# Kernel optimization log

Hardware: AMD Instinct MI355X
Metric: run time of the kernel (lower is better)

The kernel has to match this reference:

```python
import jax, jax.numpy as jnp
import numpy as np

D_Q = 512
D_O = 256  # = d_v = d_k = d_o
N_HEAD = 8
BN_EPS = 1e-5
LEAK = 0.1


def setup_inputs() -> dict:
    key = jax.random.key(0)
    ks = jax.random.split(key, 8)
    s = 0.02
    inp = {
        "q": jax.random.normal(ks[0], (64, D_Q), dtype=jnp.float32),
        "v": jax.random.normal(ks[1], (64, D_O, 32, 32), dtype=jnp.float32),
        "w_q": jax.random.normal(ks[2], (D_O, D_Q), dtype=jnp.float32) * s,
        "b_q": jnp.zeros((D_O,), jnp.float32),
        "w_kc": jax.random.normal(ks[3], (D_O, D_O), dtype=jnp.float32) * s,
        "b_kc": jnp.zeros((D_O,), jnp.float32),
        "w_kd": jax.random.normal(ks[4], (D_O, D_O), dtype=jnp.float32) * s,
        "b_kd": jnp.zeros((D_O,), jnp.float32),
        "w_v": jax.random.normal(ks[5], (D_O, D_O), dtype=jnp.float32) * s,
        "b_v": jnp.zeros((D_O,), jnp.float32),
        "temp_c": jnp.asarray(1.0, jnp.float32),
        "temp_d": jnp.asarray(1.0, jnp.float32),
        "bn_gamma": jnp.ones((D_O,), jnp.float32),
        "bn_beta": jnp.zeros((D_O,), jnp.float32),
        "bn_mean": jnp.zeros((D_O,), jnp.float32),
        "bn_var": jnp.ones((D_O,), jnp.float32),
    }
    return inp


def _conv1x1(x, wgt, bias):
    # x: (b, c, h, w), wgt: (o, c) -> (b, o, h, w)
    return jnp.einsum('bchw,oc->bohw', x, wgt) + bias[None, :, None, None]


def reference(q, v, w_q, b_q, w_kc, b_kc, w_kd, b_kd, w_v, b_v,
              temp_c, temp_d, bn_gamma, bn_beta, bn_mean, bn_var):
    b = q.shape[0]
    _, c_v, h, w = v.shape
    n = N_HEAD
    dh = D_O // n
    hw = h * w
    residual = v

    # projections
    qv = (q @ w_q.T + b_q).reshape(b, n, dh)                      # (b, n, dh)
    kc = _conv1x1(v, w_kc, b_kc).reshape(b, n, dh, hw).transpose(0, 1, 3, 2)  # (b, n, hw, dh)
    kd = _conv1x1(v, w_kd, b_kd).reshape(b, n, dh, hw).transpose(0, 1, 3, 2)
    vp = _conv1x1(v, w_v, b_v).reshape(b, n, dh, hw).transpose(0, 1, 3, 2)

    # collect: softmax attention with query length 1
    col_logit = jnp.einsum('bnd,bnsd->bns', qv, kc) / temp_c      # (b, n, hw)
    attn_col = jax.nn.softmax(col_logit, axis=2)
    attn = jnp.einsum('bns,bnsd->bnd', attn_col, vp)              # (b, n, dh)

    # diffuse: sigmoid gate, outer product with collected vector
    dif = jax.nn.sigmoid(jnp.einsum('bnsd,bnd->bns', kd, qv) / temp_d)  # (b, n, hw)
    out = jnp.einsum('bns,bnd->bnsd', dif, attn)                  # (b, n, hw, dh)

    # faithful to torch permute(0,1,4,3,2).view: swaps h and w (requires h==w)
    out = out.reshape(b, n, h, w, dh).transpose(0, 1, 4, 3, 2).reshape(b, D_O, w, h)
    out = out + residual

    # BatchNorm2d (eval: running stats) + LeakyReLU(0.1); dropout is identity at eval
    inv = bn_gamma / jnp.sqrt(bn_var + BN_EPS)
    out = (out - bn_mean[None, :, None, None]) * inv[None, :, None, None] + bn_beta[None, :, None, None]
    out = jnp.where(out >= 0, out, LEAK * out)
    return out
```

## Files before the change

kernel.cpp:

```cpp
#include <hip/hip_runtime.h>
#include <math.h>

#define B    64
#define DQ   512
#define DO   256
#define NH   8
#define DH   32
#define HW   1024
#define NCH  4
#define CHS  256

__global__ __launch_bounds__(256) void k1_qv(const float* __restrict__ q,
                                             const float* __restrict__ w_q,
                                             const float* __restrict__ b_q,
                                             float* __restrict__ qv) {
    int cg = blockIdx.x, b = blockIdx.y;
    int t = threadIdx.x;
    int wid = t >> 6, lane = t & 63;
    const float4* qrow = reinterpret_cast<const float4*>(q + (size_t)b*DQ);
    float4 q0 = qrow[lane*2], q1 = qrow[lane*2 + 1];
    #pragma unroll
    for (int r = 0; r < 4; ++r) {
        int c = cg*16 + wid*4 + r;
        const float4* wrow = reinterpret_cast<const float4*>(w_q + (size_t)c*DQ);
        float4 w0 = wrow[lane*2], w1 = wrow[lane*2 + 1];
        float acc = q0.x*w0.x + q0.y*w0.y + q0.z*w0.z + q0.w*w0.w
                  + q1.x*w1.x + q1.y*w1.y + q1.z*w1.z + q1.w*w1.w;
        #pragma unroll
        for (int k = 32; k > 0; k >>= 1) acc += __shfl_xor(acc, k);
        if (lane == 0) qv[b*DO + c] = acc + b_q[c];
    }
}

__global__ void k2_wqk(const float* __restrict__ qv,
                       const float* __restrict__ w_kc, const float* __restrict__ b_kc,
                       const float* __restrict__ w_kd, const float* __restrict__ b_kd,
                       const float* __restrict__ temp_c, const float* __restrict__ temp_d,
                       float* __restrict__ wqkc, float* __restrict__ wqkd,
                       float* __restrict__ qbc, float* __restrict__ qbd) {
    int bn = blockIdx.x;
    int n  = bn & 7;
    int t  = threadIdx.x;
    __shared__ float qvs[DH];
    if (t < DH) qvs[t] = qv[(bn >> 3)*DO + n*DH + t];
    __syncthreads();
    float itc = 1.0f / temp_c[0];
    float itd = 1.0f / temp_d[0];
    float ac = 0.f, ad = 0.f;
    #pragma unroll
    for (int d = 0; d < DH; ++d) {
        float qd = qvs[d];
        ac += qd * w_kc[(n*DH + d)*DO + t];
        ad += qd * w_kd[(n*DH + d)*DO + t];
    }
    wqkc[bn*DO + t] = ac * itc;
    wqkd[bn*DO + t] = ad * itd;
    if (t == 0) {
        float sc = 0.f;
        for (int d = 0; d < DH; ++d) sc += qvs[d]*b_kc[n*DH + d];
        qbc[bn] = sc * itc;
    }
    if (t == 1) {
        float sd = 0.f;
        for (int d = 0; d < DH; ++d) sd += qvs[d]*b_kd[n*DH + d];
        qbd[bn] = sd * itd;
    }
}

__global__ __launch_bounds__(512)
void k3g(const float* __restrict__ v,
         const float* __restrict__ wqkc, const float* __restrict__ wqkd,
         const float* __restrict__ qbc,  const float* __restrict__ qbd,
         float* __restrict__ gate, float* __restrict__ pvp, float* __restrict__ mz) {
    __shared__ float e_lds[NH][CHS];
    int ch = blockIdx.x, b = blockIdx.y;
    int t  = threadIdx.x;
    int s0 = ch*CHS;
    int bn0 = b*NH;
    int lane = t & 63;
    int w = __builtin_amdgcn_readfirstlane(t >> 6);

    float ac0=0.f, ac1=0.f, ac2=0.f, ac3=0.f;
    float ad0=0.f, ad1=0.f, ad2=0.f, ad3=0.f;
    {
        const float* vb = v + (size_t)b*DO*HW + s0 + lane*4;
        const float* wc = wqkc + (size_t)(bn0 + w)*DO;
        const float* wd = wqkd + (size_t)(bn0 + w)*DO;
        #pragma unroll 8
        for (int c = 0; c < DO; ++c) {
            float4 v4 = *reinterpret_cast<const float4*>(vb + (size_t)c*HW);
            float wcv = wc[c];
            float wdv = wd[c];
            ac0 = fmaf(wcv, v4.x, ac0); ac1 = fmaf(wcv, v4.y, ac1);
            ac2 = fmaf(wcv, v4.z, ac2); ac3 = fmaf(wcv, v4.w, ac3);
            ad0 = fmaf(wdv, v4.x, ad0); ad1 = fmaf(wdv, v4.y, ad1);
            ad2 = fmaf(wdv, v4.z, ad2); ad3 = fmaf(wdv, v4.w, ad3);
        }
    }

    {
        float qc = qbc[bn0 + w], qd = qbd[bn0 + w];
        float g0 = 1.0f/(1.0f + __expf(-(ad0 + qd)));
        float g1 = 1.0f/(1.0f + __expf(-(ad1 + qd)));
        float g2 = 1.0f/(1.0f + __expf(-(ad2 + qd)));
        float g3 = 1.0f/(1.0f + __expf(-(ad3 + qd)));
        *reinterpret_cast<float4*>(gate + (size_t)(bn0 + w)*HW + s0 + lane*4)
            = make_float4(g0, g1, g2, g3);

        float l0 = ac0 + qc, l1 = ac1 + qc, l2 = ac2 + qc, l3 = ac3 + qc;
        float m = fmaxf(fmaxf(l0, l1), fmaxf(l2, l3));
        #pragma unroll
        for (int k = 32; k > 0; k >>= 1) m = fmaxf(m, __shfl_xor(m, k));
        float e0 = __expf(l0 - m), e1 = __expf(l1 - m), e2 = __expf(l2 - m), e3 = __expf(l3 - m);
        float z = e0 + e1 + e2 + e3;
        #pragma unroll
        for (int k = 32; k > 0; k >>= 1) z += __shfl_xor(z, k);
        *reinterpret_cast<float4*>(&e_lds[w][lane*4]) = make_float4(e0, e1, e2, e3);
        if (lane == 0) {
            float* mzp = mz + ((size_t)(b*NCH + ch)*NH + w)*2;
            mzp[0] = m; mzp[1] = z;
        }
    }
    __syncthreads();

    {
        int ng = t >> 8;
        int c  = t & 255;
        const float* vrow = v + ((size_t)(b*DO + c))*HW + s0;
        float a0 = 0.f, a1 = 0.f, a2 = 0.f, a3 = 0.f;
        #pragma unroll 4
        for (int j = 0; j < CHS/4; ++j) {
            float4 v4 = *reinterpret_cast<const float4*>(vrow + j*4);
            float4 e0 = *reinterpret_cast<const float4*>(&e_lds[ng*4+0][j*4]);
            float4 e1 = *reinterpret_cast<const float4*>(&e_lds[ng*4+1][j*4]);
            float4 e2 = *reinterpret_cast<const float4*>(&e_lds[ng*4+2][j*4]);
            float4 e3 = *reinterpret_cast<const float4*>(&e_lds[ng*4+3][j*4]);
            a0 += v4.x*e0.x + v4.y*e0.y + v4.z*e0.z + v4.w*e0.w;
            a1 += v4.x*e1.x + v4.y*e1.y + v4.z*e1.z + v4.w*e1.w;
            a2 += v4.x*e2.x + v4.y*e2.y + v4.z*e2.z + v4.w*e2.w;
            a3 += v4.x*e3.x + v4.y*e3.y + v4.z*e3.z + v4.w*e3.w;
        }
        size_t pb = ((size_t)(b*NCH + ch)*NH + ng*4)*DO + c;
        pvp[pb]        = a0;
        pvp[pb + DO]   = a1;
        pvp[pb + 2*DO] = a2;
        pvp[pb + 3*DO] = a3;
    }
}

__global__ void k4c(const float* __restrict__ pvp, const float* __restrict__ mz,
                    const float* __restrict__ w_v, const float* __restrict__ b_v,
                    float* __restrict__ attn) {
    __shared__ float scale[NCH][NH];
    __shared__ float pv_lds[NH*DO];
    int b = blockIdx.x, t = threadIdx.x;
    if (t < NH) {
        int n = t;
        float M = -1e30f;
        for (int ch = 0; ch < NCH; ++ch)
            M = fmaxf(M, mz[((size_t)(b*NCH+ch)*NH+n)*2]);
        float Z = 0.f;
        for (int ch = 0; ch < NCH; ++ch) {
            float sc = __expf(mz[((size_t)(b*NCH+ch)*NH+n)*2] - M);
            Z += sc * mz[((size_t)(b*NCH+ch)*NH+n)*2 + 1];
            scale[ch][n] = sc;
        }
        float inv = 1.0f/Z;
        for (int ch = 0; ch < NCH; ++ch) scale[ch][n] *= inv;
    }
    __syncthreads();
    #pragma unroll
    for (int r = 0; r < 2; ++r) {
        int i4 = t + r*256;
        int n  = i4 >> 6;
        float4 s = make_float4(0.f, 0.f, 0.f, 0.f);
        #pragma unroll
        for (int ch = 0; ch < NCH; ++ch) {
            float sc = scale[ch][n];
            float4 p = reinterpret_cast<const float4*>(pvp + (size_t)(b*NCH + ch)*NH*DO)[i4];
            s.x = fmaf(sc, p.x, s.x); s.y = fmaf(sc, p.y, s.y);
            s.z = fmaf(sc, p.z, s.z); s.w = fmaf(sc, p.w, s.w);
        }
        *reinterpret_cast<float4*>(&pv_lds[i4*4]) = s;
    }
    __syncthreads();
    int n = t >> 5;
    float acc = b_v[t];
    const float4* w4 = reinterpret_cast<const float4*>(w_v + t*DO);
    #pragma unroll 4
    for (int c4 = 0; c4 < DO/4; ++c4) {
        float4 wv = w4[c4];
        int c = c4*4;
        acc += pv_lds[n*DO+c]*wv.x + pv_lds[n*DO+c+1]*wv.y + pv_lds[n*DO+c+2]*wv.z + pv_lds[n*DO+c+3]*wv.w;
    }
    attn[b*DO + t] = acc;
}

__global__ void k5_out(const float* __restrict__ v, const float* __restrict__ gate,
                       const float* __restrict__ attn,
                       const float* __restrict__ bn_g, const float* __restrict__ bn_b,
                       const float* __restrict__ bn_m, const float* __restrict__ bn_v,
                       float* __restrict__ out) {
    int c = blockIdx.x, b = blockIdx.y;
    int n = c >> 5, d = c & 31;
    int t = threadIdx.x;
    __shared__ float g[32*33];
    float4 gv = reinterpret_cast<const float4*>(gate + (b*NH + n)*HW)[t];
    int s0 = t*4;
    int ga = s0 >> 5, gb = s0 & 31;
    g[ga*33 + gb + 0] = gv.x;
    g[ga*33 + gb + 1] = gv.y;
    g[ga*33 + gb + 2] = gv.z;
    g[ga*33 + gb + 3] = gv.w;
    __syncthreads();
    float av   = attn[(b*NH + n)*DH + d];
    float inv  = bn_g[c] / sqrtf(bn_v[c] + 1e-5f);
    float mean = bn_m[c], beta = bn_b[c];
    size_t base = ((size_t)(b*DO + c))*HW;
    float4 r4 = reinterpret_cast<const float4*>(v + base)[t];
    int l = 4*t;
    int i_ = l >> 5, j_ = l & 31;
    float x0 = g[(j_+0)*33 + i_]*av + r4.x;
    float x1 = g[(j_+1)*33 + i_]*av + r4.y;
    float x2 = g[(j_+2)*33 + i_]*av + r4.z;
    float x3 = g[(j_+3)*33 + i_]*av + r4.w;
    float y0 = (x0 - mean)*inv + beta; y0 = y0 >= 0.f ? y0 : 0.1f*y0;
    float y1 = (x1 - mean)*inv + beta; y1 = y1 >= 0.f ? y1 : 0.1f*y1;
    float y2 = (x2 - mean)*inv + beta; y2 = y2 >= 0.f ? y2 : 0.1f*y2;
    float y3 = (x3 - mean)*inv + beta; y3 = y3 >= 0.f ? y3 : 0.1f*y3;
    reinterpret_cast<float4*>(out + base)[t] = make_float4(y0, y1, y2, y3);
}

extern "C" void kernel_launch(void* const* d_in, const int* in_sizes, int n_in,
                              void* d_out, int out_size, void* d_ws, size_t ws_size,
                              hipStream_t stream) {
    const float* q      = (const float*)d_in[0];
    const float* v      = (const float*)d_in[1];
    const float* w_q    = (const float*)d_in[2];
    const float* b_q    = (const float*)d_in[3];
    const float* w_kc   = (const float*)d_in[4];
    const float* b_kc   = (const float*)d_in[5];
    const float* w_kd   = (const float*)d_in[6];
    const float* b_kd   = (const float*)d_in[7];
    const float* w_v    = (const float*)d_in[8];
    const float* b_v    = (const float*)d_in[9];
    const float* temp_c = (const float*)d_in[10];
    const float* temp_d = (const float*)d_in[11];
    const float* bn_g   = (const float*)d_in[12];
    const float* bn_b   = (const float*)d_in[13];
    const float* bn_m   = (const float*)d_in[14];
    const float* bn_v   = (const float*)d_in[15];
    float* out = (float*)d_out;

    float* ws   = (float*)d_ws;
    float* qv   = ws;
    float* wqkc = qv   + B*DO;
    float* wqkd = wqkc + B*NH*DO;
    float* qbc  = wqkd + B*NH*DO;
    float* qbd  = qbc  + B*NH;
    float* gate = qbd  + B*NH;
    float* mz   = gate + B*NH*HW;
    float* pvp  = mz   + B*NCH*NH*2;
    float* attn = pvp  + B*NCH*NH*DO;

    k1_qv <<<dim3(16, B),    256, 0, stream>>>(q, w_q, b_q, qv);
    k2_wqk<<<B*NH,           256, 0, stream>>>(qv, w_kc, b_kc, w_kd, b_kd, temp_c, temp_d,
                                               wqkc, wqkd, qbc, qbd);
    k3g   <<<dim3(NCH, B),   512, 0, stream>>>(v, wqkc, wqkd, qbc, qbd, gate, pvp, mz);
    k4c   <<<B,              256, 0, stream>>>(pvp, mz, w_v, b_v, attn);
    k5_out<<<dim3(DO, B),    256, 0, stream>>>(v, gate, attn, bn_g, bn_b, bn_m, bn_v, out);
}
```

Measured before the change: 82.91 us.

## Split channel reduction across waves in logit kernel and halve chunk size

The logit/gate kernel is reorganized so that each wave accumulates a 32-channel slice for all eight heads, instead of one head over all 256 channels. Partial sums go to LDS and are reduced per head before the sigmoid and softmax steps. This removes the eight-fold redundant reads of the v chunk within a block. Chunks shrink to 128 positions, doubling the grid, at the cost of about 68 KB of LDS per block, which limits how many blocks fit on a CU, plus an extra barrier.

```diff
diff --git a/kernel.cpp b/kernel.cpp
--- a/kernel.cpp
+++ b/kernel.cpp
@@ -7,8 +7,8 @@
 #define NH   8
 #define DH   32
 #define HW   1024
-#define NCH  4
-#define CHS  256
+#define NCH  8
+#define CHS  128
 
 __global__ __launch_bounds__(256) void k1_qv(const float* __restrict__ q,
                                              const float* __restrict__ w_q,
@@ -67,57 +67,76 @@
     }
 }
 
-__global__ __launch_bounds__(512)
-void k3g(const float* __restrict__ v,
+__global__ __launch_bounds__(512, 4)
+void k3h(const float* __restrict__ v,
          const float* __restrict__ wqkc, const float* __restrict__ wqkd,
          const float* __restrict__ qbc,  const float* __restrict__ qbd,
          float* __restrict__ gate, float* __restrict__ pvp, float* __restrict__ mz) {
+    __shared__ float pc[8*NH*CHS];
+    __shared__ float pd[8*NH*CHS];
     __shared__ float e_lds[NH][CHS];
     int ch = blockIdx.x, b = blockIdx.y;
     int t  = threadIdx.x;
     int s0 = ch*CHS;
     int bn0 = b*NH;
     int lane = t & 63;
-    int w = __builtin_amdgcn_readfirstlane(t >> 6);
-
-    float ac0=0.f, ac1=0.f, ac2=0.f, ac3=0.f;
-    float ad0=0.f, ad1=0.f, ad2=0.f, ad3=0.f;
+    int sl2  = lane*2;
+    int csub = __builtin_amdgcn_readfirstlane(t >> 6);
+
     {
-        const float* vb = v + (size_t)b*DO*HW + s0 + lane*4;
-        const float* wc = wqkc + (size_t)(bn0 + w)*DO;
-        const float* wd = wqkd + (size_t)(bn0 + w)*DO;
+        const float* vb = v + (size_t)b*DO*HW + s0 + sl2;
+        const float* wc = wqkc + (size_t)bn0*DO;
+        const float* wd = wqkd + (size_t)bn0*DO;
+        float acc_c0[NH] = {0,0,0,0,0,0,0,0}, acc_c1[NH] = {0,0,0,0,0,0,0,0};
+        float acc_d0[NH] = {0,0,0,0,0,0,0,0}, acc_d1[NH] = {0,0,0,0,0,0,0,0};
+        int cbase = csub*32;
         #pragma unroll 8
-        for (int c = 0; c < DO; ++c) {
-            float4 v4 = *reinterpret_cast<const float4*>(vb + (size_t)c*HW);
-            float wcv = wc[c];
-            float wdv = wd[c];
-            ac0 = fmaf(wcv, v4.x, ac0); ac1 = fmaf(wcv, v4.y, ac1);
-            ac2 = fmaf(wcv, v4.z, ac2); ac3 = fmaf(wcv, v4.w, ac3);
-            ad0 = fmaf(wdv, v4.x, ad0); ad1 = fmaf(wdv, v4.y, ad1);
-            ad2 = fmaf(wdv, v4.z, ad2); ad3 = fmaf(wdv, v4.w, ad3);
-        }
-    }
+        for (int cc = 0; cc < 32; ++cc) {
+            int c = cbase + cc;
+            float2 v2 = *reinterpret_cast<const float2*>(vb + (size_t)c*HW);
+            #pragma unroll
+            for (int n = 0; n < NH; ++n) {
+                float wcv = wc[n*DO + c];
+                float wdv = wd[n*DO + c];
+                acc_c0[n] = fmaf(wcv, v2.x, acc_c0[n]);
+                acc_c1[n] = fmaf(wcv, v2.y, acc_c1[n]);
+                acc_d0[n] = fmaf(wdv, v2.x, acc_d0[n]);
+                acc_d1[n] = fmaf(wdv, v2.y, acc_d1[n]);
+            }
+        }
+        #pragma unroll
+        for (int n = 0; n < NH; ++n) {
+            *reinterpret_cast<float2*>(&pc[(csub*NH + n)*CHS + sl2]) = make_float2(acc_c0[n], acc_c1[n]);
+            *reinterpret_cast<float2*>(&pd[(csub*NH + n)*CHS + sl2]) = make_float2(acc_d0[n], acc_d1[n]);
+        }
+    }
+    __syncthreads();
 
     {
-        float qc = qbc[bn0 + w], qd = qbd[bn0 + w];
-        float g0 = 1.0f/(1.0f + __expf(-(ad0 + qd)));
-        float g1 = 1.0f/(1.0f + __expf(-(ad1 + qd)));
-        float g2 = 1.0f/(1.0f + __expf(-(ad2 + qd)));
-        float g3 = 1.0f/(1.0f + __expf(-(ad3 + qd)));
-        *reinterpret_cast<float4*>(gate + (size_t)(bn0 + w)*HW + s0 + lane*4)
-            = make_float4(g0, g1, g2, g3);
-
-        float l0 = ac0 + qc, l1 = ac1 + qc, l2 = ac2 + qc, l3 = ac3 + qc;
-        float m = fmaxf(fmaxf(l0, l1), fmaxf(l2, l3));
+        int n = csub;
+        float lc0 = qbc[bn0+n], lc1 = lc0;
+        float ld0 = qbd[bn0+n], ld1 = ld0;
+        #pragma unroll
+        for (int k = 0; k < 8; ++k) {
+            float2 c2 = *reinterpret_cast<const float2*>(&pc[(k*NH + n)*CHS + sl2]);
+            float2 d2 = *reinterpret_cast<const float2*>(&pd[(k*NH + n)*CHS + sl2]);
+            lc0 += c2.x; lc1 += c2.y;
+            ld0 += d2.x; ld1 += d2.y;
+        }
+        float g0 = 1.0f/(1.0f + __expf(-ld0));
+        float g1 = 1.0f/(1.0f + __expf(-ld1));
+        *reinterpret_cast<float2*>(gate + (size_t)(bn0+n)*HW + s0 + sl2) = make_float2(g0, g1);
+
+        float m = fmaxf(lc0, lc1);
         #pragma unroll
         for (int k = 32; k > 0; k >>= 1) m = fmaxf(m, __shfl_xor(m, k));
-        float e0 = __expf(l0 - m), e1 = __expf(l1 - m), e2 = __expf(l2 - m), e3 = __expf(l3 - m);
-        float z = e0 + e1 + e2 + e3;
+        float e0 = __expf(lc0 - m), e1 = __expf(lc1 - m);
+        float z = e0 + e1;
         #pragma unroll
         for (int k = 32; k > 0; k >>= 1) z += __shfl_xor(z, k);
-        *reinterpret_cast<float4*>(&e_lds[w][lane*4]) = make_float4(e0, e1, e2, e3);
+        *reinterpret_cast<float2*>(&e_lds[n][sl2]) = make_float2(e0, e1);
         if (lane == 0) {
-            float* mzp = mz + ((size_t)(b*NCH + ch)*NH + w)*2;
+            float* mzp = mz + ((size_t)(b*NCH + ch)*NH + n)*2;
             mzp[0] = m; mzp[1] = z;
         }
     }
@@ -266,7 +285,7 @@
     k1_qv <<<dim3(16, B),    256, 0, stream>>>(q, w_q, b_q, qv);
     k2_wqk<<<B*NH,           256, 0, stream>>>(qv, w_kc, b_kc, w_kd, b_kd, temp_c, temp_d,
                                                wqkc, wqkd, qbc, qbd);
-    k3g   <<<dim3(NCH, B),   512, 0, stream>>>(v, wqkc, wqkd, qbc, qbd, gate, pvp, mz);
+    k3h   <<<dim3(NCH, B),   512, 0, stream>>>(v, wqkc, wqkd, qbc, qbd, gate, pvp, mz);
     k4c   <<<B,              256, 0, stream>>>(pvp, mz, w_v, b_v, attn);
     k5_out<<<dim3(DO, B),    256, 0, stream>>>(v, gate, attn, bn_g, bn_b, bn_m, bn_v, out);
 }
```

Measured after the change: 77.41 us. 1.07x faster.

## Stage v channel tiles through double-buffered LDS and split spatial chunks finer

Applied to the files above, without the earlier changes.

The logit kernel now splits each batch's spatial dimension into 16 chunks of 64 instead of 4 of 256, giving 1024 blocks instead of 256 so more blocks can occupy the GPU. Each block loads v in 32-channel tiles into a double-buffered shared-memory array and prefetches the next tile while computing on the current one, so each v element is read from global memory once per block instead of once per wave. Each thread now handles one spatial position rather than four. The cost is a barrier per channel tile, more partial results for k4c to combine, and a tighter launch bound that may limit registers.

```diff
diff --git a/kernel.cpp b/kernel.cpp
--- a/kernel.cpp
+++ b/kernel.cpp
@@ -7,8 +7,10 @@
 #define NH   8
 #define DH   32
 #define HW   1024
-#define NCH  4
-#define CHS  256
+#define NCH  16
+#define CHS  64
+#define CG   32
+#define NT   (DO/CG)
 
 __global__ __launch_bounds__(256) void k1_qv(const float* __restrict__ q,
                                              const float* __restrict__ w_q,
@@ -67,11 +69,12 @@
     }
 }
 
-__global__ __launch_bounds__(512)
-void k3g(const float* __restrict__ v,
+__global__ __launch_bounds__(512, 8)
+void k3i(const float* __restrict__ v,
          const float* __restrict__ wqkc, const float* __restrict__ wqkd,
          const float* __restrict__ qbc,  const float* __restrict__ qbd,
          float* __restrict__ gate, float* __restrict__ pvp, float* __restrict__ mz) {
+    __shared__ float buf[2][CG][CHS];
     __shared__ float e_lds[NH][CHS];
     int ch = blockIdx.x, b = blockIdx.y;
     int t  = threadIdx.x;
@@ -80,42 +83,47 @@
     int lane = t & 63;
     int w = __builtin_amdgcn_readfirstlane(t >> 6);
 
-    float ac0=0.f, ac1=0.f, ac2=0.f, ac3=0.f;
-    float ad0=0.f, ad1=0.f, ad2=0.f, ad3=0.f;
+    int srow = t >> 4, sc4 = (t & 15)*4;
+    const float* vb = v + (size_t)b*DO*HW + s0;
+
     {
-        const float* vb = v + (size_t)b*DO*HW + s0 + lane*4;
-        const float* wc = wqkc + (size_t)(bn0 + w)*DO;
-        const float* wd = wqkd + (size_t)(bn0 + w)*DO;
-        #pragma unroll 8
-        for (int c = 0; c < DO; ++c) {
-            float4 v4 = *reinterpret_cast<const float4*>(vb + (size_t)c*HW);
-            float wcv = wc[c];
-            float wdv = wd[c];
-            ac0 = fmaf(wcv, v4.x, ac0); ac1 = fmaf(wcv, v4.y, ac1);
-            ac2 = fmaf(wcv, v4.z, ac2); ac3 = fmaf(wcv, v4.w, ac3);
-            ad0 = fmaf(wdv, v4.x, ad0); ad1 = fmaf(wdv, v4.y, ad1);
-            ad2 = fmaf(wdv, v4.z, ad2); ad3 = fmaf(wdv, v4.w, ad3);
-        }
+        float4 st = *reinterpret_cast<const float4*>(vb + (size_t)srow*HW + sc4);
+        *reinterpret_cast<float4*>(&buf[0][srow][sc4]) = st;
+    }
+    __syncthreads();
+
+    float lc = qbc[bn0 + w];
+    float ld = qbd[bn0 + w];
+    const float* wcn = wqkc + (size_t)(bn0 + w)*DO;
+    const float* wdn = wqkd + (size_t)(bn0 + w)*DO;
+    #pragma unroll
+    for (int g = 0; g < NT; ++g) {
+        int cur = g & 1;
+        float4 nx;
+        if (g < NT-1)
+            nx = *reinterpret_cast<const float4*>(vb + (size_t)((g+1)*CG + srow)*HW + sc4);
+        int cbase = g*CG;
+        #pragma unroll
+        for (int cc = 0; cc < CG; ++cc) {
+            float vv = buf[cur][cc][lane];
+            lc = fmaf(wcn[cbase + cc], vv, lc);
+            ld = fmaf(wdn[cbase + cc], vv, ld);
+        }
+        if (g < NT-1)
+            *reinterpret_cast<float4*>(&buf[cur ^ 1][srow][sc4]) = nx;
+        __syncthreads();
     }
 
     {
-        float qc = qbc[bn0 + w], qd = qbd[bn0 + w];
-        float g0 = 1.0f/(1.0f + __expf(-(ad0 + qd)));
-        float g1 = 1.0f/(1.0f + __expf(-(ad1 + qd)));
-        float g2 = 1.0f/(1.0f + __expf(-(ad2 + qd)));
-        float g3 = 1.0f/(1.0f + __expf(-(ad3 + qd)));
-        *reinterpret_cast<float4*>(gate + (size_t)(bn0 + w)*HW + s0 + lane*4)
-            = make_float4(g0, g1, g2, g3);
-
-        float l0 = ac0 + qc, l1 = ac1 + qc, l2 = ac2 + qc, l3 = ac3 + qc;
-        float m = fmaxf(fmaxf(l0, l1), fmaxf(l2, l3));
+        gate[(size_t)(bn0 + w)*HW + s0 + lane] = 1.0f/(1.0f + __expf(-ld));
+        float m = lc;
         #pragma unroll
         for (int k = 32; k > 0; k >>= 1) m = fmaxf(m, __shfl_xor(m, k));
-        float e0 = __expf(l0 - m), e1 = __expf(l1 - m), e2 = __expf(l2 - m), e3 = __expf(l3 - m);
-        float z = e0 + e1 + e2 + e3;
+        float e = __expf(lc - m);
+        e_lds[w][lane] = e;
+        float z = e;
         #pragma unroll
         for (int k = 32; k > 0; k >>= 1) z += __shfl_xor(z, k);
-        *reinterpret_cast<float4*>(&e_lds[w][lane*4]) = make_float4(e0, e1, e2, e3);
         if (lane == 0) {
             float* mzp = mz + ((size_t)(b*NCH + ch)*NH + w)*2;
             mzp[0] = m; mzp[1] = z;
@@ -128,7 +136,7 @@
         int c  = t & 255;
         const float* vrow = v + ((size_t)(b*DO + c))*HW + s0;
         float a0 = 0.f, a1 = 0.f, a2 = 0.f, a3 = 0.f;
-        #pragma unroll 4
+        #pragma unroll
         for (int j = 0; j < CHS/4; ++j) {
             float4 v4 = *reinterpret_cast<const float4*>(vrow + j*4);
             float4 e0 = *reinterpret_cast<const float4*>(&e_lds[ng*4+0][j*4]);
@@ -266,7 +274,7 @@
     k1_qv <<<dim3(16, B),    256, 0, stream>>>(q, w_q, b_q, qv);
     k2_wqk<<<B*NH,           256, 0, stream>>>(qv, w_kc, b_kc, w_kd, b_kd, temp_c, temp_d,
                                                wqkc, wqkd, qbc, qbd);
-    k3g   <<<dim3(NCH, B),   512, 0, stream>>>(v, wqkc, wqkd, qbc, qbd, gate, pvp, mz);
+    k3i   <<<dim3(NCH, B),   512, 0, stream>>>(v, wqkc, wqkd, qbc, qbd, gate, pvp, mz);
     k4c   <<<B,              256, 0, stream>>>(pvp, mz, w_v, b_v, attn);
     k5_out<<<dim3(DO, B),    256, 0, stream>>>(v, gate, attn, bn_g, bn_b, bn_m, bn_v, out);
 }
```

New measurement: 81.26 us. 1.02x faster.

## Stage v chunk in swizzled LDS and split spatial axis into smaller chunks

Applied to the files above, without the earlier changes.

The main fused kernel now loads a 256x64 tile of v into shared memory once, with an XOR swizzle, and reuses it for both the key-logit and the value-accumulation passes. Before, v was read from global memory twice. The spatial chunk shrinks from 256 to 64 (16 chunks), which multiplies the block count by four so more CUs are busy. Each wave splits the channel loop across four lane groups and reduces them with shuffles. The two per-head weight vectors are interleaved into one float2 buffer. The cost is more partial results for the combine kernel and 72KB of LDS per block.

```diff
diff --git a/kernel.cpp b/kernel.cpp
--- a/kernel.cpp
+++ b/kernel.cpp
@@ -7,8 +7,8 @@
 #define NH   8
 #define DH   32
 #define HW   1024
-#define NCH  4
-#define CHS  256
+#define NCH  16
+#define CHS  64
 
 __global__ __launch_bounds__(256) void k1_qv(const float* __restrict__ q,
                                              const float* __restrict__ w_q,
@@ -36,13 +36,14 @@
                        const float* __restrict__ w_kc, const float* __restrict__ b_kc,
                        const float* __restrict__ w_kd, const float* __restrict__ b_kd,
                        const float* __restrict__ temp_c, const float* __restrict__ temp_d,
-                       float* __restrict__ wqkc, float* __restrict__ wqkd,
-                       float* __restrict__ qbc, float* __restrict__ qbd) {
+                       float* __restrict__ wpack, float* __restrict__ qbc,
+                       float* __restrict__ qbd) {
     int bn = blockIdx.x;
     int n  = bn & 7;
+    int bb = bn >> 3;
     int t  = threadIdx.x;
     __shared__ float qvs[DH];
-    if (t < DH) qvs[t] = qv[(bn >> 3)*DO + n*DH + t];
+    if (t < DH) qvs[t] = qv[bb*DO + n*DH + t];
     __syncthreads();
     float itc = 1.0f / temp_c[0];
     float itd = 1.0f / temp_d[0];
@@ -53,8 +54,8 @@
         ac += qd * w_kc[(n*DH + d)*DO + t];
         ad += qd * w_kd[(n*DH + d)*DO + t];
     }
-    wqkc[bn*DO + t] = ac * itc;
-    wqkd[bn*DO + t] = ad * itd;
+    wpack[((size_t)bn*DO + t)*2 + 0] = ac * itc;
+    wpack[((size_t)bn*DO + t)*2 + 1] = ad * itd;
     if (t == 0) {
         float sc = 0.f;
         for (int d = 0; d < DH; ++d) sc += qvs[d]*b_kc[n*DH + d];
@@ -67,11 +68,12 @@
     }
 }
 
-__global__ __launch_bounds__(512)
-void k3g(const float* __restrict__ v,
-         const float* __restrict__ wqkc, const float* __restrict__ wqkd,
+__global__ __launch_bounds__(512, 2)
+void k3r(const float* __restrict__ v,
+         const float* __restrict__ wpack,
          const float* __restrict__ qbc,  const float* __restrict__ qbd,
          float* __restrict__ gate, float* __restrict__ pvp, float* __restrict__ mz) {
+    __shared__ float vbuf[DO][CHS];
     __shared__ float e_lds[NH][CHS];
     int ch = blockIdx.x, b = blockIdx.y;
     int t  = threadIdx.x;
@@ -80,42 +82,65 @@
     int lane = t & 63;
     int w = __builtin_amdgcn_readfirstlane(t >> 6);
 
+    {
+        int s4 = t & 15, srow = t >> 4;
+        const float* vb = v + (size_t)b*DO*HW + s0;
+        int idx4 = (s4 ^ (srow & 15)) * 4;
+        #pragma unroll
+        for (int k = 0; k < 8; ++k) {
+            float4 r = *reinterpret_cast<const float4*>(vb + (size_t)(k*32+srow)*HW + s4*4);
+            *reinterpret_cast<float4*>(&vbuf[k*32+srow][idx4]) = r;
+        }
+    }
+    __syncthreads();
+
     float ac0=0.f, ac1=0.f, ac2=0.f, ac3=0.f;
     float ad0=0.f, ad1=0.f, ad2=0.f, ad3=0.f;
     {
-        const float* vb = v + (size_t)b*DO*HW + s0 + lane*4;
-        const float* wc = wqkc + (size_t)(bn0 + w)*DO;
-        const float* wd = wqkd + (size_t)(bn0 + w)*DO;
+        int c_off = lane >> 4, s4 = lane & 15;
+        const float2* wp = reinterpret_cast<const float2*>(wpack) + (size_t)(bn0 + w)*DO;
         #pragma unroll 8
-        for (int c = 0; c < DO; ++c) {
-            float4 v4 = *reinterpret_cast<const float4*>(vb + (size_t)c*HW);
-            float wcv = wc[c];
-            float wdv = wd[c];
-            ac0 = fmaf(wcv, v4.x, ac0); ac1 = fmaf(wcv, v4.y, ac1);
-            ac2 = fmaf(wcv, v4.z, ac2); ac3 = fmaf(wcv, v4.w, ac3);
-            ad0 = fmaf(wdv, v4.x, ad0); ad1 = fmaf(wdv, v4.y, ad1);
-            ad2 = fmaf(wdv, v4.z, ad2); ad3 = fmaf(wdv, v4.w, ad3);
-        }
-    }
-
-    {
+        for (int cc = 0; cc < 64; ++cc) {
+            int c = cc*4 + c_off;
+            float4 v4 = *reinterpret_cast<const float4*>(&vbuf[c][(s4 ^ (c & 15))*4]);
+            float2 wv = wp[c];
+            ac0 = fmaf(wv.x, v4.x, ac0); ac1 = fmaf(wv.x, v4.y, ac1);
+            ac2 = fmaf(wv.x, v4.z, ac2); ac3 = fmaf(wv.x, v4.w, ac3);
+            ad0 = fmaf(wv.y, v4.x, ad0); ad1 = fmaf(wv.y, v4.y, ad1);
+            ad2 = fmaf(wv.y, v4.z, ad2); ad3 = fmaf(wv.y, v4.w, ad3);
+        }
+        ac0 += __shfl_xor(ac0, 16); ac0 += __shfl_xor(ac0, 32);
+        ac1 += __shfl_xor(ac1, 16); ac1 += __shfl_xor(ac1, 32);
+        ac2 += __shfl_xor(ac2, 16); ac2 += __shfl_xor(ac2, 32);
+        ac3 += __shfl_xor(ac3, 16); ac3 += __shfl_xor(ac3, 32);
+        ad0 += __shfl_xor(ad0, 16); ad0 += __shfl_xor(ad0, 32);
+        ad1 += __shfl_xor(ad1, 16); ad1 += __shfl_xor(ad1, 32);
+        ad2 += __shfl_xor(ad2, 16); ad2 += __shfl_xor(ad2, 32);
+        ad3 += __shfl_xor(ad3, 16); ad3 += __shfl_xor(ad3, 32);
+    }
+
+    {
+        int s4 = lane & 15;
         float qc = qbc[bn0 + w], qd = qbd[bn0 + w];
+        float l0 = ac0 + qc, l1 = ac1 + qc, l2 = ac2 + qc, l3 = ac3 + qc;
         float g0 = 1.0f/(1.0f + __expf(-(ad0 + qd)));
         float g1 = 1.0f/(1.0f + __expf(-(ad1 + qd)));
         float g2 = 1.0f/(1.0f + __expf(-(ad2 + qd)));
         float g3 = 1.0f/(1.0f + __expf(-(ad3 + qd)));
-        *reinterpret_cast<float4*>(gate + (size_t)(bn0 + w)*HW + s0 + lane*4)
-            = make_float4(g0, g1, g2, g3);
-
-        float l0 = ac0 + qc, l1 = ac1 + qc, l2 = ac2 + qc, l3 = ac3 + qc;
+        if (lane < 16)
+            *reinterpret_cast<float4*>(gate + (size_t)(bn0 + w)*HW + s0 + s4*4)
+                = make_float4(g0, g1, g2, g3);
+
         float m = fmaxf(fmaxf(l0, l1), fmaxf(l2, l3));
         #pragma unroll
-        for (int k = 32; k > 0; k >>= 1) m = fmaxf(m, __shfl_xor(m, k));
-        float e0 = __expf(l0 - m), e1 = __expf(l1 - m), e2 = __expf(l2 - m), e3 = __expf(l3 - m);
+        for (int k = 1; k <= 8; k <<= 1) m = fmaxf(m, __shfl_xor(m, k));
+        float e0 = __expf(l0 - m), e1 = __expf(l1 - m);
+        float e2 = __expf(l2 - m), e3 = __expf(l3 - m);
         float z = e0 + e1 + e2 + e3;
         #pragma unroll
-        for (int k = 32; k > 0; k >>= 1) z += __shfl_xor(z, k);
-        *reinterpret_cast<float4*>(&e_lds[w][lane*4]) = make_float4(e0, e1, e2, e3);
+        for (int k = 1; k <= 8; k <<= 1) z += __shfl_xor(z, k);
+        if (lane < 16)
+            *reinterpret_cast<float4*>(&e_lds[w][s4*4]) = make_float4(e0, e1, e2, e3);
         if (lane == 0) {
             float* mzp = mz + ((size_t)(b*NCH + ch)*NH + w)*2;
             mzp[0] = m; mzp[1] = z;
@@ -124,23 +149,22 @@
     __syncthreads();
 
     {
-        int ng = t >> 8;
-        int c  = t & 255;
-        const float* vrow = v + ((size_t)(b*DO + c))*HW + s0;
+        int c = t & 255, nh = t >> 8;
+        int cx = c & 15;
         float a0 = 0.f, a1 = 0.f, a2 = 0.f, a3 = 0.f;
-        #pragma unroll 4
-        for (int j = 0; j < CHS/4; ++j) {
-            float4 v4 = *reinterpret_cast<const float4*>(vrow + j*4);
-            float4 e0 = *reinterpret_cast<const float4*>(&e_lds[ng*4+0][j*4]);
-            float4 e1 = *reinterpret_cast<const float4*>(&e_lds[ng*4+1][j*4]);
-            float4 e2 = *reinterpret_cast<const float4*>(&e_lds[ng*4+2][j*4]);
-            float4 e3 = *reinterpret_cast<const float4*>(&e_lds[ng*4+3][j*4]);
+        #pragma unroll
+        for (int j = 0; j < 16; ++j) {
+            float4 v4 = *reinterpret_cast<const float4*>(&vbuf[c][(j ^ cx)*4]);
+            float4 e0 = *reinterpret_cast<const float4*>(&e_lds[nh*4+0][j*4]);
+            float4 e1 = *reinterpret_cast<const float4*>(&e_lds[nh*4+1][j*4]);
+            float4 e2 = *reinterpret_cast<const float4*>(&e_lds[nh*4+2][j*4]);
+            float4 e3 = *reinterpret_cast<const float4*>(&e_lds[nh*4+3][j*4]);
             a0 += v4.x*e0.x + v4.y*e0.y + v4.z*e0.z + v4.w*e0.w;
             a1 += v4.x*e1.x + v4.y*e1.y + v4.z*e1.z + v4.w*e1.w;
             a2 += v4.x*e2.x + v4.y*e2.y + v4.z*e2.z + v4.w*e2.w;
             a3 += v4.x*e3.x + v4.y*e3.y + v4.z*e3.z + v4.w*e3.w;
         }
-        size_t pb = ((size_t)(b*NCH + ch)*NH + ng*4)*DO + c;
+        size_t pb = ((size_t)(b*NCH + ch)*NH + nh*4)*DO + c;
         pvp[pb]        = a0;
         pvp[pb + DO]   = a1;
         pvp[pb + 2*DO] = a2;
@@ -174,7 +198,7 @@
         int i4 = t + r*256;
         int n  = i4 >> 6;
         float4 s = make_float4(0.f, 0.f, 0.f, 0.f);
-        #pragma unroll
+        #pragma unroll 4
         for (int ch = 0; ch < NCH; ++ch) {
             float sc = scale[ch][n];
             float4 p = reinterpret_cast<const float4*>(pvp + (size_t)(b*NCH + ch)*NH*DO)[i4];
@@ -252,21 +276,20 @@
     const float* bn_v   = (const float*)d_in[15];
     float* out = (float*)d_out;
 
-    float* ws   = (float*)d_ws;
-    float* qv   = ws;
-    float* wqkc = qv   + B*DO;
-    float* wqkd = wqkc + B*NH*DO;
-    float* qbc  = wqkd + B*NH*DO;
-    float* qbd  = qbc  + B*NH;
-    float* gate = qbd  + B*NH;
-    float* mz   = gate + B*NH*HW;
-    float* pvp  = mz   + B*NCH*NH*2;
-    float* attn = pvp  + B*NCH*NH*DO;
+    float* ws    = (float*)d_ws;
+    float* qv    = ws;
+    float* wpack = qv    + B*DO;
+    float* qbc   = wpack + (size_t)B*NH*DO*2;
+    float* qbd   = qbc   + B*NH;
+    float* gate  = qbd   + B*NH;
+    float* mz    = gate  + B*NH*HW;
+    float* pvp   = mz    + B*NCH*NH*2;
+    float* attn  = pvp   + (size_t)B*NCH*NH*DO;
 
     k1_qv <<<dim3(16, B),    256, 0, stream>>>(q, w_q, b_q, qv);
     k2_wqk<<<B*NH,           256, 0, stream>>>(qv, w_kc, b_kc, w_kd, b_kd, temp_c, temp_d,
-                                               wqkc, wqkd, qbc, qbd);
-    k3g   <<<dim3(NCH, B),   512, 0, stream>>>(v, wqkc, wqkd, qbc, qbd, gate, pvp, mz);
+                                               wpack, qbc, qbd);
+    k3r   <<<dim3(NCH, B),   512, 0, stream>>>(v, wpack, qbc, qbd, gate, pvp, mz);
     k4c   <<<B,              256, 0, stream>>>(pvp, mz, w_v, b_v, attn);
     k5_out<<<dim3(DO, B),    256, 0, stream>>>(v, gate, attn, bn_g, bn_b, bn_m, bn_v, out);
 }
```

Result: faster. 78.53 us (-5.3%).
